# Kernel tuning notes

Hardware: AMD Instinct MI355X
Metric: run time of the kernel (lower is better)

Reference implementation:

```python
import jax, jax.numpy as jnp
import numpy as np

B, T, Dx, H, K = 32, 4096, 128, 128, 10


def setup_inputs() -> dict:
    key = jax.random.key(0)
    ks = jax.random.split(key, 11)
    s = 1.0 / np.sqrt(H)  # PyTorch GRU init range

    def p(k, shape):
        return jax.random.uniform(k, shape, jnp.float32, -s, s)

    return {
        "x": jax.random.normal(ks[0], (B, T, Dx), jnp.float32),
        # forward-direction GRU params (gate order: r, z, n as in PyTorch)
        "W_ih_f": p(ks[1], (3 * H, Dx)),
        "W_hh_f": p(ks[2], (3 * H, H)),
        "b_ih_f": p(ks[3], (3 * H,)),
        "b_hh_f": p(ks[4], (3 * H,)),
        # backward-direction GRU params
        "W_ih_b": p(ks[5], (3 * H, Dx)),
        "W_hh_b": p(ks[6], (3 * H, H)),
        "b_ih_b": p(ks[7], (3 * H,)),
        "b_hh_b": p(ks[8], (3 * H,)),
        # final linear classifier
        "W_fc": p(ks[9], (K, 2 * H)),
        "b_fc": p(ks[10], (K,)),
    }


def _gru_scan(x, Wih, Whh, bih, bhh, reverse):
    """Single-direction GRU over time. x: [B,T,Dx] -> [B,T,H]."""
    # Precompute all input projections at once: [T, B, 3H]
    xp = jnp.einsum('btd,gd->tbg', x, Wih) + bih
    Whh_T = Whh.T
    Hd = Whh.shape[1]

    def cell(h, xt):
        hp = h @ Whh_T + bhh            # [B, 3H]
        xr, xz, xn = jnp.split(xt, 3, axis=-1)
        hr, hz, hn = jnp.split(hp, 3, axis=-1)
        r = jax.nn.sigmoid(xr + hr)
        z = jax.nn.sigmoid(xz + hz)
        n = jnp.tanh(xn + r * hn)
        h_new = (1.0 - z) * n + z * h
        return h_new, h_new

    h0 = jnp.zeros((x.shape[0], Hd), x.dtype)
    _, hs = jax.lax.scan(cell, h0, xp, reverse=reverse)  # [T, B, H]
    return jnp.transpose(hs, (1, 0, 2))


def reference(x, W_ih_f, W_hh_f, b_ih_f, b_hh_f,
              W_ih_b, W_hh_b, b_ih_b, b_hh_b, W_fc, b_fc):
    hf = _gru_scan(x, W_ih_f, W_hh_f, b_ih_f, b_hh_f, reverse=False)
    hb = _gru_scan(x, W_ih_b, W_hh_b, b_ih_b, b_hh_b, reverse=True)
    h = jnp.concatenate([hf, hb], axis=-1)  # [B, T, 2H]
    return h @ W_fc.T + b_fc                # [B, T, K]
```

## Files before the change

kernel.cpp:

```cpp
#include <hip/hip_runtime.h>
#include <cstdint>
#include <cstddef>

#define T_LEN   4096
#define B_SZ    32
#define H_DIM   128
#define DX      128
#define K_CLS   10
#define CHUNK   32
#define NCHUNKS (T_LEN / CHUNK)
#define XA_LD   136
#define XP_LD   520
#define HI_LD   136

typedef _Float16 half2v  __attribute__((ext_vector_type(2)));
typedef _Float16 half4   __attribute__((ext_vector_type(4)));
typedef _Float16 half8   __attribute__((ext_vector_type(8)));
typedef float    floatx4 __attribute__((ext_vector_type(4)));

#define LGKM_BARRIER() do {                                   \
    asm volatile("s_waitcnt lgkmcnt(0)" ::: "memory");        \
    __builtin_amdgcn_s_barrier();                             \
    asm volatile("" ::: "memory");                            \
  } while (0)

__global__ void __launch_bounds__(256) init_out_kernel(float* __restrict__ out,
                                                       const float* __restrict__ bfc) {
  int i = blockIdx.x * 256 + threadIdx.x;
  if (i < B_SZ * T_LEN * K_CLS) out[i] = bfc[i % K_CLS];
}

__global__ void __launch_bounds__(512, 2)
gru_bidir_kernel(const float* __restrict__ x,
                 const float* __restrict__ Wih_f, const float* __restrict__ Whh_f,
                 const float* __restrict__ bih_f, const float* __restrict__ bhh_f,
                 const float* __restrict__ Wih_b, const float* __restrict__ Whh_b,
                 const float* __restrict__ bih_b, const float* __restrict__ bhh_b,
                 const float* __restrict__ Wfc, float* __restrict__ out) {
  const int tid = threadIdx.x;
  const int bid = blockIdx.x;
  const int b   = bid & (B_SZ - 1);
  const int dir = bid >> 5;

  const float* Wih = dir ? Wih_b : Wih_f;
  const float* Whh = dir ? Whh_b : Whh_f;
  const float* bih = dir ? bih_b : bih_f;
  const float* bhh = dir ? bhh_b : bhh_f;

  const int lane = tid & 63;
  const int wv   = tid >> 6;
  const int col  = lane & 15;
  const int quad = lane >> 4;
  const int jloc = wv * 16 + col;

  __shared__ __align__(16) _Float16 xA[CHUNK][XA_LD];
  __shared__ __align__(16) _Float16 xPL[CHUNK][XP_LD];
  __shared__ __align__(16) _Float16 hist[CHUNK + 1][HI_LD];

  const float LOG2E = 1.44269504f;

  half8 whf[3][4];
  half8 wif[3][4];
#pragma unroll
  for (int g = 0; g < 3; ++g) {
    const float gs = (g == 2) ? 2.0f * LOG2E : LOG2E;
#pragma unroll
    for (int kt = 0; kt < 4; ++kt) {
      const float* sh = Whh + (size_t)(g * H_DIM + jloc) * H_DIM + kt * 32 + quad * 8;
      const float* si = Wih + (size_t)(g * H_DIM + jloc) * DX + kt * 32 + quad * 8;
      half8 vh, vi;
#pragma unroll
      for (int e = 0; e < 8; ++e) {
        vh[e] = (_Float16)(sh[e] * gs);
        vi[e] = (_Float16)(si[e] * gs);
      }
      whf[g][kt] = vh;
      wif[g][kt] = vi;
    }
  }
  const float bias_r = (bih[jloc] + bhh[jloc]) * LOG2E;
  const float bias_z = (bih[H_DIM + jloc] + bhh[H_DIM + jloc]) * LOG2E;
  const float bias_n = bih[2 * H_DIM + jloc] * (2.0f * LOG2E);
  const float bhn_s  = bhh[2 * H_DIM + jloc] * (2.0f * LOG2E);

  half8 fcf[4];
  if (wv < 2) {
#pragma unroll
    for (int kt = 0; kt < 4; ++kt) {
      half8 v;
#pragma unroll
      for (int e = 0; e < 8; ++e) {
        int k = kt * 32 + quad * 8 + e;
        v[e] = (col < K_CLS) ? (_Float16)Wfc[(size_t)col * (2 * H_DIM) + dir * H_DIM + k]
                             : (_Float16)0.f;
      }
      fcf[kt] = v;
    }
  }

  half8 hz;
#pragma unroll
  for (int e = 0; e < 8; ++e) hz[e] = (_Float16)0.f;
  half8 haf0 = hz, haf1 = hz, haf2 = hz, haf3 = hz;

  if (tid < H_DIM) hist[0][tid] = (_Float16)0.f;

  const int s_row = tid >> 4;
  const int cb    = (tid & 15) * 8;
  float4 px0, px1;
  {
    int t0 = dir ? (T_LEN - 1 - s_row) : s_row;
    const float* xr = x + ((size_t)b * T_LEN + t0) * DX + cb;
    px0 = *(const float4*)xr;
    px1 = *(const float4*)(xr + 4);
  }

  float hold = 0.f;
  const floatx4 z4 = {0.f, 0.f, 0.f, 0.f};
  __syncthreads();

  for (int c = 0; c < NCHUNKS; ++c) {
    {
      half8 v;
      v[0] = (_Float16)px0.x; v[1] = (_Float16)px0.y; v[2] = (_Float16)px0.z; v[3] = (_Float16)px0.w;
      v[4] = (_Float16)px1.x; v[5] = (_Float16)px1.y; v[6] = (_Float16)px1.z; v[7] = (_Float16)px1.w;
      *(half8*)&xA[s_row][cb] = v;
    }
    LGKM_BARRIER();

#pragma unroll
    for (int mt = 0; mt < 2; ++mt) {
      half8 af[4];
#pragma unroll
      for (int kt = 0; kt < 4; ++kt)
        af[kt] = *(const half8*)&xA[mt * 16 + col][kt * 32 + quad * 8];
      floatx4 pr = z4, pz = z4, pn = z4;
#pragma unroll
      for (int kt = 0; kt < 4; ++kt) {
        pr = __builtin_amdgcn_mfma_f32_16x16x32_f16(af[kt], wif[0][kt], pr, 0, 0, 0);
        pz = __builtin_amdgcn_mfma_f32_16x16x32_f16(af[kt], wif[1][kt], pz, 0, 0, 0);
        pn = __builtin_amdgcn_mfma_f32_16x16x32_f16(af[kt], wif[2][kt], pn, 0, 0, 0);
      }
#pragma unroll
      for (int i = 0; i < 4; ++i) {
        half4 w;
        w[0] = (_Float16)(pr[i] + bias_r);
        w[1] = (_Float16)(pz[i] + bias_z);
        w[2] = (_Float16)(pn[i] + bias_n);
        w[3] = (_Float16)0.f;
        *(half4*)&xPL[mt * 16 + quad * 4 + i][jloc * 4] = w;
      }
    }

    if (c + 1 < NCHUNKS) {
      int s  = (c + 1) * CHUNK + s_row;
      int t0 = dir ? (T_LEN - 1 - s) : s;
      const float* xr = x + ((size_t)b * T_LEN + t0) * DX + cb;
      px0 = *(const float4*)xr;
      px1 = *(const float4*)(xr + 4);
    }
    LGKM_BARRIER();

    uint2 xv = *(const uint2*)&xPL[0][jloc * 4];

#pragma unroll 2
    for (int s = 0; s < CHUNK; ++s) {
      if (col == 0) {
        haf0 = *(const half8*)&hist[s][quad * 8];
        haf1 = *(const half8*)&hist[s][32 + quad * 8];
        haf2 = *(const half8*)&hist[s][64 + quad * 8];
        haf3 = *(const half8*)&hist[s][96 + quad * 8];
      }
      uint2 xvn = *(const uint2*)&xPL[(s + 1) & (CHUNK - 1)][jloc * 4];

      floatx4 cr0 = __builtin_amdgcn_mfma_f32_16x16x32_f16(haf0, whf[0][0], z4, 0, 0, 0);
      floatx4 cr1 = __builtin_amdgcn_mfma_f32_16x16x32_f16(haf1, whf[0][1], z4, 0, 0, 0);
      floatx4 cr2 = __builtin_amdgcn_mfma_f32_16x16x32_f16(haf2, whf[0][2], z4, 0, 0, 0);
      floatx4 cr3 = __builtin_amdgcn_mfma_f32_16x16x32_f16(haf3, whf[0][3], z4, 0, 0, 0);
      floatx4 cz0 = __builtin_amdgcn_mfma_f32_16x16x32_f16(haf0, whf[1][0], z4, 0, 0, 0);
      floatx4 cz1 = __builtin_amdgcn_mfma_f32_16x16x32_f16(haf1, whf[1][1], z4, 0, 0, 0);
      floatx4 cz2 = __builtin_amdgcn_mfma_f32_16x16x32_f16(haf2, whf[1][2], z4, 0, 0, 0);
      floatx4 cz3 = __builtin_amdgcn_mfma_f32_16x16x32_f16(haf3, whf[1][3], z4, 0, 0, 0);
      floatx4 cn0 = __builtin_amdgcn_mfma_f32_16x16x32_f16(haf0, whf[2][0], z4, 0, 0, 0);
      floatx4 cn1 = __builtin_amdgcn_mfma_f32_16x16x32_f16(haf1, whf[2][1], z4, 0, 0, 0);
      floatx4 cn2 = __builtin_amdgcn_mfma_f32_16x16x32_f16(haf2, whf[2][2], z4, 0, 0, 0);
      floatx4 cn3 = __builtin_amdgcn_mfma_f32_16x16x32_f16(haf3, whf[2][3], z4, 0, 0, 0);

      float ar = (cr0[0] + cr1[0]) + (cr2[0] + cr3[0]);
      float az = (cz0[0] + cz1[0]) + (cz2[0] + cz3[0]);
      float an = (cn0[0] + cn1[0]) + (cn2[0] + cn3[0]);

      half2v x01 = __builtin_bit_cast(half2v, xv.x);
      half2v x23 = __builtin_bit_cast(half2v, xv.y);

      float rr = __builtin_amdgcn_rcpf(1.f + __builtin_amdgcn_exp2f(-((float)x01.x + ar)));
      float zz = __builtin_amdgcn_rcpf(1.f + __builtin_amdgcn_exp2f(-((float)x01.y + az)));
      float yn = fmaf(rr, an + bhn_s, (float)x23.x);
      float t  = __builtin_amdgcn_exp2f(-fmaxf(yn, -80.f));
      float nn = (1.f - t) * __builtin_amdgcn_rcpf(1.f + t);
      hold = nn + zz * (hold - nn);

      if (quad == 0) hist[s + 1][jloc] = (_Float16)hold;
      LGKM_BARRIER();
      xv = xvn;
    }

    if (wv < 2) {
      floatx4 fa = z4;
#pragma unroll
      for (int kt = 0; kt < 4; ++kt) {
        half8 af = *(const half8*)&hist[1 + wv * 16 + col][kt * 32 + quad * 8];
        fa = __builtin_amdgcn_mfma_f32_16x16x32_f16(af, fcf[kt], fa, 0, 0, 0);
      }
      if (col < K_CLS) {
#pragma unroll
        for (int i = 0; i < 4; ++i) {
          int t  = c * CHUNK + wv * 16 + quad * 4 + i;
          int tt = dir ? (T_LEN - 1 - t) : t;
          atomicAdd(out + ((size_t)b * T_LEN + tt) * K_CLS + col, fa[i]);
        }
      }
    }
    if (tid >= 256 && tid < 256 + H_DIM) hist[0][tid - 256] = hist[CHUNK][tid - 256];
  }
}

extern "C" void kernel_launch(void* const* d_in, const int* in_sizes, int n_in,
                              void* d_out, int out_size, void* d_ws, size_t ws_size,
                              hipStream_t stream) {
  (void)in_sizes; (void)n_in; (void)d_ws; (void)ws_size; (void)out_size;
  const float* x     = (const float*)d_in[0];
  const float* Wih_f = (const float*)d_in[1];
  const float* Whh_f = (const float*)d_in[2];
  const float* bih_f = (const float*)d_in[3];
  const float* bhh_f = (const float*)d_in[4];
  const float* Wih_b = (const float*)d_in[5];
  const float* Whh_b = (const float*)d_in[6];
  const float* bih_b = (const float*)d_in[7];
  const float* bhh_b = (const float*)d_in[8];
  const float* Wfc   = (const float*)d_in[9];
  const float* bfc   = (const float*)d_in[10];
  float* out = (float*)d_out;

  const int n_out = B_SZ * T_LEN * K_CLS;
  init_out_kernel<<<(n_out + 255) / 256, 256, 0, stream>>>(out, bfc);
  gru_bidir_kernel<<<B_SZ * 2, 512, 0, stream>>>(x, Wih_f, Whh_f, bih_f, bhh_f,
                                                 Wih_b, Whh_b, bih_b, bhh_b, Wfc, out);
}
```

Measured before the change: 1.724 ms.

## Halve GRU block to 4 waves, each computing two hidden-unit column tiles

Shrinks the per-direction block from 8 waves to 4. Each wave now holds weights for two 16-column tiles and runs 24 MFMAs per step, so the per-step barrier synchronises fewer waves. It also folds the input projection and the hidden bias into the MFMA accumulator init, and fully unrolls the chunk loop. The cost is twice the register footprint and twice the serial MFMA chain per wave on the recurrent critical path.

```diff
diff --git a/kernel.cpp b/kernel.cpp
--- a/kernel.cpp
+++ b/kernel.cpp
@@ -30,7 +30,7 @@
   if (i < B_SZ * T_LEN * K_CLS) out[i] = bfc[i % K_CLS];
 }
 
-__global__ void __launch_bounds__(512, 2)
+__global__ void __launch_bounds__(256, 1)
 gru_bidir_kernel(const float* __restrict__ x,
                  const float* __restrict__ Wih_f, const float* __restrict__ Whh_f,
                  const float* __restrict__ bih_f, const float* __restrict__ bhh_f,
@@ -51,7 +51,8 @@
   const int wv   = tid >> 6;
   const int col  = lane & 15;
   const int quad = lane >> 4;
-  const int jloc = wv * 16 + col;
+  const int j0   = wv * 32 + col;
+  const int j1   = j0 + 16;
 
   __shared__ __align__(16) _Float16 xA[CHUNK][XA_LD];
   __shared__ __align__(16) _Float16 xPL[CHUNK][XP_LD];
@@ -59,29 +60,40 @@
 
   const float LOG2E = 1.44269504f;
 
-  half8 whf[3][4];
-  half8 wif[3][4];
-#pragma unroll
-  for (int g = 0; g < 3; ++g) {
-    const float gs = (g == 2) ? 2.0f * LOG2E : LOG2E;
-#pragma unroll
-    for (int kt = 0; kt < 4; ++kt) {
-      const float* sh = Whh + (size_t)(g * H_DIM + jloc) * H_DIM + kt * 32 + quad * 8;
-      const float* si = Wih + (size_t)(g * H_DIM + jloc) * DX + kt * 32 + quad * 8;
-      half8 vh, vi;
-#pragma unroll
-      for (int e = 0; e < 8; ++e) {
-        vh[e] = (_Float16)(sh[e] * gs);
-        vi[e] = (_Float16)(si[e] * gs);
-      }
-      whf[g][kt] = vh;
-      wif[g][kt] = vi;
-    }
-  }
-  const float bias_r = (bih[jloc] + bhh[jloc]) * LOG2E;
-  const float bias_z = (bih[H_DIM + jloc] + bhh[H_DIM + jloc]) * LOG2E;
-  const float bias_n = bih[2 * H_DIM + jloc] * (2.0f * LOG2E);
-  const float bhn_s  = bhh[2 * H_DIM + jloc] * (2.0f * LOG2E);
+  half8 whf[2][3][4];
+  half8 wif[2][3][4];
+#pragma unroll
+  for (int ct = 0; ct < 2; ++ct) {
+    const int jct = wv * 32 + ct * 16 + col;
+#pragma unroll
+    for (int g = 0; g < 3; ++g) {
+      const float gs = (g == 2) ? 2.0f * LOG2E : LOG2E;
+#pragma unroll
+      for (int kt = 0; kt < 4; ++kt) {
+        const float* sh = Whh + (size_t)(g * H_DIM + jct) * H_DIM + kt * 32 + quad * 8;
+        const float* si = Wih + (size_t)(g * H_DIM + jct) * DX + kt * 32 + quad * 8;
+        half8 vh, vi;
+#pragma unroll
+        for (int e = 0; e < 8; ++e) {
+          vh[e] = (_Float16)(sh[e] * gs);
+          vi[e] = (_Float16)(si[e] * gs);
+        }
+        whf[ct][g][kt] = vh;
+        wif[ct][g][kt] = vi;
+      }
+    }
+  }
+  float br[2], bz[2], bn[2];
+  floatx4 cNbv[2];
+#pragma unroll
+  for (int ct = 0; ct < 2; ++ct) {
+    const int jct = wv * 32 + ct * 16 + col;
+    br[ct] = (bih[jct] + bhh[jct]) * LOG2E;
+    bz[ct] = (bih[H_DIM + jct] + bhh[H_DIM + jct]) * LOG2E;
+    bn[ct] = bih[2 * H_DIM + jct] * (2.0f * LOG2E);
+    float bh = bhh[2 * H_DIM + jct] * (2.0f * LOG2E);
+    cNbv[ct] = (floatx4){bh, bh, bh, bh};
+  }
 
   half8 fcf[4];
   if (wv < 2) {
@@ -98,33 +110,31 @@
     }
   }
 
-  half8 hz;
-#pragma unroll
-  for (int e = 0; e < 8; ++e) hz[e] = (_Float16)0.f;
-  half8 haf0 = hz, haf1 = hz, haf2 = hz, haf3 = hz;
-
   if (tid < H_DIM) hist[0][tid] = (_Float16)0.f;
 
-  const int s_row = tid >> 4;
-  const int cb    = (tid & 15) * 8;
-  float4 px0, px1;
+  const int s_row = tid >> 3;
+  const int cb    = (tid & 7) * 16;
+  float4 px0, px1, px2, px3;
   {
     int t0 = dir ? (T_LEN - 1 - s_row) : s_row;
     const float* xr = x + ((size_t)b * T_LEN + t0) * DX + cb;
-    px0 = *(const float4*)xr;
-    px1 = *(const float4*)(xr + 4);
-  }
-
-  float hold = 0.f;
+    px0 = *(const float4*)xr;        px1 = *(const float4*)(xr + 4);
+    px2 = *(const float4*)(xr + 8);  px3 = *(const float4*)(xr + 12);
+  }
+
+  float hold0 = 0.f, hold1 = 0.f;
   const floatx4 z4 = {0.f, 0.f, 0.f, 0.f};
   __syncthreads();
 
   for (int c = 0; c < NCHUNKS; ++c) {
     {
-      half8 v;
-      v[0] = (_Float16)px0.x; v[1] = (_Float16)px0.y; v[2] = (_Float16)px0.z; v[3] = (_Float16)px0.w;
-      v[4] = (_Float16)px1.x; v[5] = (_Float16)px1.y; v[6] = (_Float16)px1.z; v[7] = (_Float16)px1.w;
-      *(half8*)&xA[s_row][cb] = v;
+      half8 lo, hi;
+      lo[0] = (_Float16)px0.x; lo[1] = (_Float16)px0.y; lo[2] = (_Float16)px0.z; lo[3] = (_Float16)px0.w;
+      lo[4] = (_Float16)px1.x; lo[5] = (_Float16)px1.y; lo[6] = (_Float16)px1.z; lo[7] = (_Float16)px1.w;
+      hi[0] = (_Float16)px2.x; hi[1] = (_Float16)px2.y; hi[2] = (_Float16)px2.z; hi[3] = (_Float16)px2.w;
+      hi[4] = (_Float16)px3.x; hi[5] = (_Float16)px3.y; hi[6] = (_Float16)px3.z; hi[7] = (_Float16)px3.w;
+      *(half8*)&xA[s_row][cb] = lo;
+      *(half8*)&xA[s_row][cb + 8] = hi;
     }
     LGKM_BARRIER();
 
@@ -134,21 +144,25 @@
 #pragma unroll
       for (int kt = 0; kt < 4; ++kt)
         af[kt] = *(const half8*)&xA[mt * 16 + col][kt * 32 + quad * 8];
-      floatx4 pr = z4, pz = z4, pn = z4;
-#pragma unroll
-      for (int kt = 0; kt < 4; ++kt) {
-        pr = __builtin_amdgcn_mfma_f32_16x16x32_f16(af[kt], wif[0][kt], pr, 0, 0, 0);
-        pz = __builtin_amdgcn_mfma_f32_16x16x32_f16(af[kt], wif[1][kt], pz, 0, 0, 0);
-        pn = __builtin_amdgcn_mfma_f32_16x16x32_f16(af[kt], wif[2][kt], pn, 0, 0, 0);
-      }
-#pragma unroll
-      for (int i = 0; i < 4; ++i) {
-        half4 w;
-        w[0] = (_Float16)(pr[i] + bias_r);
-        w[1] = (_Float16)(pz[i] + bias_z);
-        w[2] = (_Float16)(pn[i] + bias_n);
-        w[3] = (_Float16)0.f;
-        *(half4*)&xPL[mt * 16 + quad * 4 + i][jloc * 4] = w;
+#pragma unroll
+      for (int ct = 0; ct < 2; ++ct) {
+        floatx4 pr = z4, pz = z4, pn = z4;
+#pragma unroll
+        for (int kt = 0; kt < 4; ++kt) {
+          pr = __builtin_amdgcn_mfma_f32_16x16x32_f16(af[kt], wif[ct][0][kt], pr, 0, 0, 0);
+          pz = __builtin_amdgcn_mfma_f32_16x16x32_f16(af[kt], wif[ct][1][kt], pz, 0, 0, 0);
+          pn = __builtin_amdgcn_mfma_f32_16x16x32_f16(af[kt], wif[ct][2][kt], pn, 0, 0, 0);
+        }
+        const int jw = (ct ? j1 : j0) * 4;
+#pragma unroll
+        for (int i = 0; i < 4; ++i) {
+          half4 w;
+          w[0] = (_Float16)(pr[i] + br[ct]);
+          w[1] = (_Float16)(pz[i] + bz[ct]);
+          w[2] = (_Float16)(pn[i] + bn[ct]);
+          w[3] = (_Float16)0.f;
+          *(half4*)&xPL[mt * 16 + quad * 4 + i][jw] = w;
+        }
       }
     }
 
@@ -156,53 +170,80 @@
       int s  = (c + 1) * CHUNK + s_row;
       int t0 = dir ? (T_LEN - 1 - s) : s;
       const float* xr = x + ((size_t)b * T_LEN + t0) * DX + cb;
-      px0 = *(const float4*)xr;
-      px1 = *(const float4*)(xr + 4);
+      px0 = *(const float4*)xr;        px1 = *(const float4*)(xr + 4);
+      px2 = *(const float4*)(xr + 8);  px3 = *(const float4*)(xr + 12);
     }
     LGKM_BARRIER();
 
-    uint2 xv = *(const uint2*)&xPL[0][jloc * 4];
-
-#pragma unroll 2
+    uint2 xv0 = *(const uint2*)&xPL[0][j0 * 4];
+    uint2 xv1 = *(const uint2*)&xPL[0][j1 * 4];
+
+#pragma unroll
     for (int s = 0; s < CHUNK; ++s) {
-      if (col == 0) {
-        haf0 = *(const half8*)&hist[s][quad * 8];
-        haf1 = *(const half8*)&hist[s][32 + quad * 8];
-        haf2 = *(const half8*)&hist[s][64 + quad * 8];
-        haf3 = *(const half8*)&hist[s][96 + quad * 8];
-      }
-      uint2 xvn = *(const uint2*)&xPL[(s + 1) & (CHUNK - 1)][jloc * 4];
-
-      floatx4 cr0 = __builtin_amdgcn_mfma_f32_16x16x32_f16(haf0, whf[0][0], z4, 0, 0, 0);
-      floatx4 cr1 = __builtin_amdgcn_mfma_f32_16x16x32_f16(haf1, whf[0][1], z4, 0, 0, 0);
-      floatx4 cr2 = __builtin_amdgcn_mfma_f32_16x16x32_f16(haf2, whf[0][2], z4, 0, 0, 0);
-      floatx4 cr3 = __builtin_amdgcn_mfma_f32_16x16x32_f16(haf3, whf[0][3], z4, 0, 0, 0);
-      floatx4 cz0 = __builtin_amdgcn_mfma_f32_16x16x32_f16(haf0, whf[1][0], z4, 0, 0, 0);
-      floatx4 cz1 = __builtin_amdgcn_mfma_f32_16x16x32_f16(haf1, whf[1][1], z4, 0, 0, 0);
-      floatx4 cz2 = __builtin_amdgcn_mfma_f32_16x16x32_f16(haf2, whf[1][2], z4, 0, 0, 0);
-      floatx4 cz3 = __builtin_amdgcn_mfma_f32_16x16x32_f16(haf3, whf[1][3], z4, 0, 0, 0);
-      floatx4 cn0 = __builtin_amdgcn_mfma_f32_16x16x32_f16(haf0, whf[2][0], z4, 0, 0, 0);
-      floatx4 cn1 = __builtin_amdgcn_mfma_f32_16x16x32_f16(haf1, whf[2][1], z4, 0, 0, 0);
-      floatx4 cn2 = __builtin_amdgcn_mfma_f32_16x16x32_f16(haf2, whf[2][2], z4, 0, 0, 0);
-      floatx4 cn3 = __builtin_amdgcn_mfma_f32_16x16x32_f16(haf3, whf[2][3], z4, 0, 0, 0);
-
-      float ar = (cr0[0] + cr1[0]) + (cr2[0] + cr3[0]);
-      float az = (cz0[0] + cz1[0]) + (cz2[0] + cz3[0]);
-      float an = (cn0[0] + cn1[0]) + (cn2[0] + cn3[0]);
-
-      half2v x01 = __builtin_bit_cast(half2v, xv.x);
-      half2v x23 = __builtin_bit_cast(half2v, xv.y);
-
-      float rr = __builtin_amdgcn_rcpf(1.f + __builtin_amdgcn_exp2f(-((float)x01.x + ar)));
-      float zz = __builtin_amdgcn_rcpf(1.f + __builtin_amdgcn_exp2f(-((float)x01.y + az)));
-      float yn = fmaf(rr, an + bhn_s, (float)x23.x);
-      float t  = __builtin_amdgcn_exp2f(-fmaxf(yn, -80.f));
-      float nn = (1.f - t) * __builtin_amdgcn_rcpf(1.f + t);
-      hold = nn + zz * (hold - nn);
-
-      if (quad == 0) hist[s + 1][jloc] = (_Float16)hold;
+      half8 haf[4];
+#pragma unroll
+      for (int kt = 0; kt < 4; ++kt)
+        haf[kt] = *(const half8*)&hist[s][kt * 32 + quad * 8];
+      uint2 xvn0 = *(const uint2*)&xPL[(s + 1) & (CHUNK - 1)][j0 * 4];
+      uint2 xvn1 = *(const uint2*)&xPL[(s + 1) & (CHUNK - 1)][j1 * 4];
+
+      half2v xa0 = __builtin_bit_cast(half2v, xv0.x);
+      half2v xb0 = __builtin_bit_cast(half2v, xv0.y);
+      half2v xa1 = __builtin_bit_cast(half2v, xv1.x);
+      half2v xb1 = __builtin_bit_cast(half2v, xv1.y);
+      float xr0 = (float)xa0.x, xz0 = (float)xa0.y, xn0 = (float)xb0.x;
+      float xr1 = (float)xa1.x, xz1 = (float)xa1.y, xn1 = (float)xb1.x;
+      floatx4 cR0 = {xr0, xr0, xr0, xr0}, cZ0 = {xz0, xz0, xz0, xz0};
+      floatx4 cR1 = {xr1, xr1, xr1, xr1}, cZ1 = {xz1, xz1, xz1, xz1};
+
+      floatx4 a0[3][4], a1[3][4];
+#pragma unroll
+      for (int g = 0; g < 3; ++g) {
+#pragma unroll
+        for (int kt = 0; kt < 4; ++kt) {
+          floatx4 c0 = (kt == 0) ? ((g == 0) ? cR0 : (g == 1) ? cZ0 : cNbv[0]) : z4;
+          a0[g][kt] = __builtin_amdgcn_mfma_f32_16x16x32_f16(haf[kt], whf[0][g][kt], c0, 0, 0, 0);
+        }
+      }
+#pragma unroll
+      for (int g = 0; g < 3; ++g) {
+#pragma unroll
+        for (int kt = 0; kt < 4; ++kt) {
+          floatx4 c1 = (kt == 0) ? ((g == 0) ? cR1 : (g == 1) ? cZ1 : cNbv[1]) : z4;
+          a1[g][kt] = __builtin_amdgcn_mfma_f32_16x16x32_f16(haf[kt], whf[1][g][kt], c1, 0, 0, 0);
+        }
+      }
+
+      {
+        float ar = (a0[0][0][0] + a0[0][1][0]) + (a0[0][2][0] + a0[0][3][0]);
+        float rr = __builtin_amdgcn_rcpf(1.f + __builtin_amdgcn_exp2f(-ar));
+        float az = (a0[1][0][0] + a0[1][1][0]) + (a0[1][2][0] + a0[1][3][0]);
+        float zz = __builtin_amdgcn_rcpf(1.f + __builtin_amdgcn_exp2f(-az));
+        float an = (a0[2][0][0] + a0[2][1][0]) + (a0[2][2][0] + a0[2][3][0]);
+        float yn = fmaf(rr, an, xn0);
+        float t  = __builtin_amdgcn_exp2f(-fmaxf(yn, -80.f));
+        float nn = fmaf(2.f, __builtin_amdgcn_rcpf(1.f + t), -1.f);
+        hold0 = fmaf(zz, hold0 - nn, nn);
+      }
+      {
+        float ar = (a1[0][0][0] + a1[0][1][0]) + (a1[0][2][0] + a1[0][3][0]);
+        float rr = __builtin_amdgcn_rcpf(1.f + __builtin_amdgcn_exp2f(-ar));
+        float az = (a1[1][0][0] + a1[1][1][0]) + (a1[1][2][0] + a1[1][3][0]);
+        float zz = __builtin_amdgcn_rcpf(1.f + __builtin_amdgcn_exp2f(-az));
+        float an = (a1[2][0][0] + a1[2][1][0]) + (a1[2][2][0] + a1[2][3][0]);
+        float yn = fmaf(rr, an, xn1);
+        float t  = __builtin_amdgcn_exp2f(-fmaxf(yn, -80.f));
+        float nn = fmaf(2.f, __builtin_amdgcn_rcpf(1.f + t), -1.f);
+        hold1 = fmaf(zz, hold1 - nn, nn);
+      }
+
+      if (quad == 0) {
+        hist[s + 1][j0] = (_Float16)hold0;
+        hist[s + 1][j1] = (_Float16)hold1;
+      }
       LGKM_BARRIER();
-      xv = xvn;
+      xv0 = xvn0;
+      xv1 = xvn1;
     }
 
     if (wv < 2) {
@@ -220,8 +261,9 @@
           atomicAdd(out + ((size_t)b * T_LEN + tt) * K_CLS + col, fa[i]);
         }
       }
-    }
-    if (tid >= 256 && tid < 256 + H_DIM) hist[0][tid - 256] = hist[CHUNK][tid - 256];
+    } else if (wv == 2) {
+      ((unsigned int*)&hist[0][0])[lane] = ((const unsigned int*)&hist[CHUNK][0])[lane];
+    }
   }
 }
 
@@ -244,6 +286,6 @@
 
   const int n_out = B_SZ * T_LEN * K_CLS;
   init_out_kernel<<<(n_out + 255) / 256, 256, 0, stream>>>(out, bfc);
-  gru_bidir_kernel<<<B_SZ * 2, 512, 0, stream>>>(x, Wih_f, Whh_f, bih_f, bhh_f,
+  gru_bidir_kernel<<<B_SZ * 2, 256, 0, stream>>>(x, Wih_f, Whh_f, bih_f, bhh_f,
                                                  Wih_b, Whh_b, bih_b, bhh_b, Wfc, out);
 }
```

After: 2.001 ms. 16.0% more time.
